# Performance work log

Hardware: AMD Instinct MI355X
Metric: run time of the kernel (lower is better)

## Reference

```python
import jax, jax.numpy as jnp
import numpy as np

DIM = 1024
NUM_HEADS = 16
HEAD_DIM = DIM // NUM_HEADS


def setup_inputs() -> dict:
    key = jax.random.key(0)
    k_x, k_wqkv, k_bqkv, k_wo, k_bo = jax.random.split(key, 5)
    scale = DIM ** -0.5
    return {
        "x": jax.random.normal(k_x, (4, 2048, DIM), dtype=jnp.float32),
        "w_qkv": jax.random.normal(k_wqkv, (DIM, 3 * DIM), dtype=jnp.float32) * scale,
        "b_qkv": jax.random.normal(k_bqkv, (3 * DIM,), dtype=jnp.float32) * 0.02,
        "w_out": jax.random.normal(k_wo, (DIM, DIM), dtype=jnp.float32) * scale,
        "b_out": jax.random.normal(k_bo, (DIM,), dtype=jnp.float32) * 0.02,
    }


def reference(x, w_qkv, b_qkv, w_out, b_out):
    B, S, D = x.shape
    H, Hd = NUM_HEADS, HEAD_DIM
    # QKV projection: (B,S,3D) -> (3,B,H,S,Hd)
    qkv = (x @ w_qkv + b_qkv).reshape(B, S, 3, H, Hd).transpose(2, 0, 3, 1, 4)
    q, k, v = qkv[0], qkv[1], qkv[2]
    scores = jnp.einsum('bhqd,bhkd->bhqk', q, k) / (Hd ** 0.5)
    attn = jax.nn.softmax(scores, axis=-1)  # dropout is identity in eval
    out = jnp.einsum('bhqk,bhkd->bhqd', attn, v)
    out = out.transpose(0, 2, 1, 3).reshape(B, S, D)
    return out @ w_out + b_out
```

## Files before the change

kernel.cpp:

```cpp
#include <hip/hip_runtime.h>
#include <hip/hip_bf16.h>
#include <stdint.h>

#define SEQ 2048
#define DIM 1024
#define NH 16
#define HD 64

typedef __attribute__((ext_vector_type(8))) short short8;
typedef __attribute__((ext_vector_type(4))) float f32x4;
typedef __attribute__((ext_vector_type(4))) float float4v;
typedef __attribute__((ext_vector_type(4))) unsigned short u16x4;
typedef __attribute__((ext_vector_type(2))) unsigned int u32x2;

#define MFMA16(a, b, c) __builtin_amdgcn_mfma_f32_16x16x32_bf16(a, b, c, 0, 0, 0)

#define QSCALE 0.1803368801111244f
#define LOG2_THR 11.0f

__device__ __forceinline__ unsigned short f2b(float f) {
  union { float f; unsigned int u; } x; x.f = f;
  unsigned int r = (x.u + 0x7FFFu + ((x.u >> 16) & 1u)) >> 16;
  return (unsigned short)r;
}

__device__ __forceinline__ float exp2v(float x) {
  float r;
  asm("v_exp_f32 %0, %1" : "=v"(r) : "v"(x));
  return r;
}

__device__ __forceinline__ unsigned int pk2(float a, float b) {
  __hip_bfloat162 h = __float22bfloat162_rn(float2{a, b});
  union { __hip_bfloat162 h; unsigned int u; } c; c.h = h;
  return c.u;
}

__device__ __forceinline__ void gld16(const void* g, void* l) {
  __builtin_amdgcn_global_load_lds(
      (const __attribute__((address_space(1))) unsigned int*)(uintptr_t)g,
      (__attribute__((address_space(3))) unsigned int*)(unsigned int)(uintptr_t)l,
      16, 0, 0);
}

__global__ void cast_bf16_kernel(const float* __restrict__ in,
                                 unsigned short* __restrict__ out, int n4) {
  int stride = gridDim.x * blockDim.x;
  for (int i = blockIdx.x * blockDim.x + threadIdx.x; i < n4; i += stride) {
    float4v v = *(const float4v*)(in + (size_t)i * 4);
    u16x4 o;
    o.x = f2b(v.x); o.y = f2b(v.y); o.z = f2b(v.z); o.w = f2b(v.w);
    *(u16x4*)(out + (size_t)i * 4) = o;
  }
}

__global__ void transpose_cast_kernel(const float* __restrict__ in,
                                      unsigned short* __restrict__ out,
                                      int rows, int cols) {
  __shared__ float tile[32][33];
  const int t = threadIdx.x, tx = t & 31, ty = t >> 5;
  const int c0 = blockIdx.x * 32, r0 = blockIdx.y * 32;
#pragma unroll
  for (int j = 0; j < 4; j++)
    tile[ty + 8 * j][tx] = in[(size_t)(r0 + ty + 8 * j) * cols + c0 + tx];
  __syncthreads();
#pragma unroll
  for (int j = 0; j < 4; j++)
    out[(size_t)(c0 + ty + 8 * j) * rows + r0 + tx] = f2b(tile[tx][ty + 8 * j]);
}

template <int EPI>
__global__ __launch_bounds__(256, 2) void gemm_bt_kernel(
    const unsigned short* __restrict__ A, const unsigned short* __restrict__ Bt,
    const float* __restrict__ bias, float* __restrict__ Cf,
    int M, int N, int K,
    unsigned short* __restrict__ Qb, unsigned short* __restrict__ Kb,
    unsigned short* __restrict__ Vt) {
  __shared__ unsigned short lA[128 * 32];
  __shared__ unsigned short lB[128 * 32];
  const int t = threadIdx.x, lane = t & 63, w = t >> 6;
  const int l15 = lane & 15, lg = lane >> 4;
  const int wr = (w >> 1) * 64, wc = (w & 1) * 64;
  const int bm = blockIdx.x, bn = blockIdx.y;
  const char* Ag = (const char*)(A + (size_t)bm * 128 * K);
  const char* Bg = (const char*)(Bt + (size_t)bn * 128 * K);
  const int sr = t >> 2;
  const int sc = (t & 3) * 16;
  const size_t rowb = (size_t)K * 2;

  f32x4 acc[4][4];
#pragma unroll
  for (int m = 0; m < 4; m++)
#pragma unroll
    for (int n = 0; n < 4; n++) acc[m][n] = (f32x4){0.f, 0.f, 0.f, 0.f};

  for (int k0 = 0; k0 < K; k0 += 32) {
    __syncthreads();
    const size_t kbyte = (size_t)k0 * 2;
    gld16(Ag + (size_t)sr * rowb + kbyte + sc, &lA[t * 8]);
    gld16(Ag + (size_t)(sr + 64) * rowb + kbyte + sc, &lA[2048 + t * 8]);
    gld16(Bg + (size_t)sr * rowb + kbyte + sc, &lB[t * 8]);
    gld16(Bg + (size_t)(sr + 64) * rowb + kbyte + sc, &lB[2048 + t * 8]);
    asm volatile("s_waitcnt vmcnt(0)" ::: "memory");
    __syncthreads();
    short8 af[4], bf_[4];
#pragma unroll
    for (int m = 0; m < 4; m++)
      af[m] = *(const short8*)&lA[(wr + m * 16 + l15) * 32 + lg * 8];
#pragma unroll
    for (int n = 0; n < 4; n++)
      bf_[n] = *(const short8*)&lB[(wc + n * 16 + l15) * 32 + lg * 8];
#pragma unroll
    for (int m = 0; m < 4; m++)
#pragma unroll
      for (int n = 0; n < 4; n++)
        acc[m][n] = MFMA16(af[m], bf_[n], acc[m][n]);
  }

#pragma unroll
  for (int m = 0; m < 4; m++) {
#pragma unroll
    for (int n = 0; n < 4; n++) {
      const int row0 = bm * 128 + wr + m * 16 + lg * 4;
      const int col = bn * 128 + wc + n * 16 + l15;
      const float bv = bias[col];
      if (EPI == 1) {
#pragma unroll
        for (int rr = 0; rr < 4; rr++)
          Cf[(size_t)(row0 + rr) * N + col] = acc[m][n][rr] + bv;
      } else {
        const int three = col >> 10, rem = col & 1023;
        const int h = rem >> 6, d = rem & 63;
        const int b = row0 >> 11, s0 = row0 & 2047;
        const size_t bh = (size_t)(b * NH + h);
        if (three == 0) {
#pragma unroll
          for (int rr = 0; rr < 4; rr++)
            Qb[(bh * SEQ + s0 + rr) * HD + d] = f2b((acc[m][n][rr] + bv) * QSCALE);
        } else if (three == 1) {
#pragma unroll
          for (int rr = 0; rr < 4; rr++)
            Kb[(bh * SEQ + s0 + rr) * HD + d] = f2b(acc[m][n][rr] + bv);
        } else {
          u16x4 pk;
#pragma unroll
          for (int rr = 0; rr < 4; rr++) pk[rr] = f2b(acc[m][n][rr] + bv);
          *(u16x4*)&Vt[(bh * HD + d) * SEQ + s0] = pk;
        }
      }
    }
  }
}

__global__ __launch_bounds__(256, 3) void attn_kernel(
    const unsigned short* __restrict__ Qb, const unsigned short* __restrict__ Kb,
    const unsigned short* __restrict__ Vt, unsigned short* __restrict__ AO) {
  __shared__ unsigned short kT[2][64 * 64];
  __shared__ unsigned short vT[2][64 * 64];
  __shared__ unsigned short pT[4][32 * 64];
  const int t = threadIdx.x, lane = t & 63, w = t >> 6;
  const int l15 = lane & 15, lg = lane >> 4;
  const int flat = blockIdx.y * 16 + blockIdx.x;
  const int xcd = flat & 7, j = flat >> 3;
  const int bh = xcd * 8 + (j >> 4);
  const int q0 = (j & 15) * 128;
  const char* Qg = (const char*)(Qb + (size_t)bh * SEQ * HD);
  const char* Kg = (const char*)(Kb + (size_t)bh * SEQ * HD);
  const char* Vg = (const char*)(Vt + (size_t)bh * HD * SEQ);

  short8 qa[2][2];
#pragma unroll
  for (int h = 0; h < 2; h++) {
    const char* qrow = Qg + (size_t)(q0 + w * 32 + h * 16 + l15) * 128;
    qa[h][0] = *(const short8*)(qrow + lg * 16);
    qa[h][1] = *(const short8*)(qrow + 64 + lg * 16);
  }

  f32x4 o[2][4];
#pragma unroll
  for (int h = 0; h < 2; h++)
#pragma unroll
    for (int n = 0; n < 4; n++) o[h][n] = (f32x4){0.f, 0.f, 0.f, 0.f};
  float m_r[2] = {-1e30f, -1e30f}, l_r[2] = {0.f, 0.f};

  const int sr0 = t >> 3;
  const int scx = (t & 7) * 16;

#define STAGE(buf, kv0_)                                                               \
  do {                                                                                 \
    const int r0_ = sr0, r1_ = sr0 + 32;                                               \
    gld16(Kg + (size_t)((kv0_) + r0_) * 128 + (scx ^ ((r0_ & 7) << 4)),                \
          &kT[buf][t * 8]);                                                            \
    gld16(Kg + (size_t)((kv0_) + r1_) * 128 + (scx ^ ((r1_ & 7) << 4)),                \
          &kT[buf][2048 + t * 8]);                                                     \
    gld16(Vg + (size_t)r0_ * (SEQ * 2) + (size_t)(kv0_) * 2 + (scx ^ ((r0_ & 7) << 4)),\
          &vT[buf][t * 8]);                                                            \
    gld16(Vg + (size_t)r1_ * (SEQ * 2) + (size_t)(kv0_) * 2 + (scx ^ ((r1_ & 7) << 4)),\
          &vT[buf][2048 + t * 8]);                                                     \
  } while (0)

  STAGE(0, 0);
  asm volatile("s_waitcnt vmcnt(0)" ::: "memory");
  __syncthreads();
  int cur = 0;

  for (int kv0 = 0; kv0 < SEQ; kv0 += 64) {
    if (kv0 + 64 < SEQ) STAGE(cur ^ 1, kv0 + 64);

    const char* kb = (const char*)&kT[cur][0];
    f32x4 s[2][4];
#pragma unroll
    for (int h = 0; h < 2; h++)
#pragma unroll
      for (int n = 0; n < 4; n++) s[h][n] = (f32x4){0.f, 0.f, 0.f, 0.f};
    __builtin_amdgcn_s_setprio(1);
#pragma unroll
    for (int n = 0; n < 4; n++) {
      const int row = n * 16 + l15;
      const char* kr = kb + row * 128;
      const int sw = (row & 7) << 4;
      short8 a0 = *(const short8*)(kr + ((lg * 16) ^ sw));
      short8 a1 = *(const short8*)(kr + ((64 + lg * 16) ^ sw));
      s[0][n] = MFMA16(a0, qa[0][0], s[0][n]);
      s[0][n] = MFMA16(a1, qa[0][1], s[0][n]);
      s[1][n] = MFMA16(a0, qa[1][0], s[1][n]);
      s[1][n] = MFMA16(a1, qa[1][1], s[1][n]);
    }
    __builtin_amdgcn_s_setprio(0);

    float mx[2];
#pragma unroll
    for (int h = 0; h < 2; h++) {
      float m0 = fmaxf(fmaxf(s[h][0][0], s[h][0][1]), fmaxf(s[h][0][2], s[h][0][3]));
#pragma unroll
      for (int n = 1; n < 4; n++) {
        m0 = fmaxf(m0, fmaxf(fmaxf(s[h][n][0], s[h][n][1]), fmaxf(s[h][n][2], s[h][n][3])));
      }
      m0 = fmaxf(m0, __shfl_xor(m0, 16, 64));
      m0 = fmaxf(m0, __shfl_xor(m0, 32, 64));
      mx[h] = m0;
    }

    const int grow = (mx[0] > m_r[0] + LOG2_THR) | (mx[1] > m_r[1] + LOG2_THR);
    if (__any(grow)) {
      float al[2];
#pragma unroll
      for (int h = 0; h < 2; h++) {
        const float nm = fmaxf(m_r[h], mx[h]);
        al[h] = exp2v(m_r[h] - nm);
        m_r[h] = nm;
        l_r[h] *= al[h];
      }
#pragma unroll
      for (int h = 0; h < 2; h++)
#pragma unroll
        for (int r = 0; r < 4; r++) {
          const float alb = __shfl(al[h], lg * 4 + r, 64);
#pragma unroll
          for (int n = 0; n < 4; n++) o[h][n][r] *= alb;
        }
    }

    char* pb = (char*)&pT[w][0];
    const int swp = (l15 & 7) << 4;
#pragma unroll
    for (int h = 0; h < 2; h++) {
      float rs = 0.f;
#pragma unroll
      for (int n = 0; n < 4; n++) {
#pragma unroll
        for (int r = 0; r < 4; r++) {
          const float p = exp2v(s[h][n][r] - m_r[h]);
          s[h][n][r] = p;
          rs += p;
        }
        u32x2 c;
        c.x = pk2(s[h][n][0], s[h][n][1]);
        c.y = pk2(s[h][n][2], s[h][n][3]);
        *(u32x2*)(pb + (h * 16 + l15) * 128 + ((n * 32 + lg * 8) ^ swp)) = c;
      }
      rs += __shfl_xor(rs, 16, 64);
      rs += __shfl_xor(rs, 32, 64);
      l_r[h] += rs;
    }
    short8 pa[2][2];
#pragma unroll
    for (int h = 0; h < 2; h++) {
      const char* pr = pb + (h * 16 + l15) * 128;
      pa[h][0] = *(const short8*)(pr + ((lg * 16) ^ swp));
      pa[h][1] = *(const short8*)(pr + ((64 + lg * 16) ^ swp));
    }

    const char* vb = (const char*)&vT[cur][0];
    __builtin_amdgcn_s_setprio(1);
#pragma unroll
    for (int n = 0; n < 4; n++) {
      const int row = n * 16 + l15;
      const char* vr = vb + row * 128;
      const int sw = (row & 7) << 4;
      short8 b0 = *(const short8*)(vr + ((lg * 16) ^ sw));
      short8 b1 = *(const short8*)(vr + ((64 + lg * 16) ^ sw));
      o[0][n] = MFMA16(pa[0][0], b0, o[0][n]);
      o[0][n] = MFMA16(pa[0][1], b1, o[0][n]);
      o[1][n] = MFMA16(pa[1][0], b0, o[1][n]);
      o[1][n] = MFMA16(pa[1][1], b1, o[1][n]);
    }
    __builtin_amdgcn_s_setprio(0);

    asm volatile("s_waitcnt vmcnt(0)" ::: "memory");
    __syncthreads();
    cur ^= 1;
  }
#undef STAGE

  float inv[2];
#pragma unroll
  for (int h = 0; h < 2; h++) inv[h] = 1.f / l_r[h];
  const int b = bh >> 4, hh = bh & 15;
  unsigned short* aob = AO + (size_t)b * SEQ * DIM + (size_t)hh * HD;
#pragma unroll
  for (int h = 0; h < 2; h++)
#pragma unroll
    for (int r = 0; r < 4; r++) {
      const float lb = __shfl(inv[h], lg * 4 + r, 64);
      const int s_ = q0 + w * 32 + h * 16 + lg * 4 + r;
#pragma unroll
      for (int n = 0; n < 4; n++) {
        const int d_ = n * 16 + l15;
        aob[(size_t)s_ * DIM + d_] = f2b(o[h][n][r] * lb);
      }
    }
}

extern "C" void kernel_launch(void* const* d_in, const int* in_sizes, int n_in,
                              void* d_out, int out_size, void* d_ws, size_t ws_size,
                              hipStream_t stream) {
  const float* x = (const float*)d_in[0];
  const float* w_qkv = (const float*)d_in[1];
  const float* b_qkv = (const float*)d_in[2];
  const float* w_out = (const float*)d_in[3];
  const float* b_out = (const float*)d_in[4];
  float* out = (float*)d_out;

  char* ws = (char*)d_ws;
  unsigned short* xb    = (unsigned short*)(ws);
  unsigned short* wqkvT = (unsigned short*)(ws + (16u << 20));
  unsigned short* woT   = (unsigned short*)(ws + (22u << 20));
  unsigned short* Qb    = (unsigned short*)(ws + (24u << 20));
  unsigned short* Kb    = (unsigned short*)(ws + (40u << 20));
  unsigned short* Vt    = (unsigned short*)(ws + (56u << 20));
  unsigned short* AO    = (unsigned short*)(ws + (72u << 20));

  const int M = 4 * SEQ;

  cast_bf16_kernel<<<2048, 256, 0, stream>>>(x, xb, M * DIM / 4);
  transpose_cast_kernel<<<dim3(3 * DIM / 32, DIM / 32), 256, 0, stream>>>(w_qkv, wqkvT, DIM, 3 * DIM);
  transpose_cast_kernel<<<dim3(DIM / 32, DIM / 32), 256, 0, stream>>>(w_out, woT, DIM, DIM);

  gemm_bt_kernel<0><<<dim3(M / 128, 3 * DIM / 128), 256, 0, stream>>>(
      xb, wqkvT, b_qkv, nullptr, M, 3 * DIM, DIM, Qb, Kb, Vt);

  attn_kernel<<<dim3(SEQ / 128, 4 * NH), 256, 0, stream>>>(Qb, Kb, Vt, AO);

  gemm_bt_kernel<1><<<dim3(M / 128, DIM / 128), 256, 0, stream>>>(
      AO, woT, b_out, out, M, DIM, DIM, nullptr, nullptr, nullptr);
}
```

Measured before the change: 300.7 us.

## Load K and V tiles directly from global memory instead of LDS staging

```diff
diff --git a/kernel.cpp b/kernel.cpp
--- a/kernel.cpp
+++ b/kernel.cpp
@@ -152,12 +152,10 @@
   }
 }
 
-__global__ __launch_bounds__(256, 3) void attn_kernel(
+__global__ __launch_bounds__(256, 4) void attn_kernel(
     const unsigned short* __restrict__ Qb, const unsigned short* __restrict__ Kb,
     const unsigned short* __restrict__ Vt, unsigned short* __restrict__ AO) {
-  __shared__ unsigned short kT[2][64 * 64];
-  __shared__ unsigned short vT[2][64 * 64];
-  __shared__ unsigned short pT[4][32 * 64];
+  __shared__ unsigned short pT[4][16 * 64];
   const int t = threadIdx.x, lane = t & 63, w = t >> 6;
   const int l15 = lane & 15, lg = lane >> 4;
   const int flat = blockIdx.y * 16 + blockIdx.x;
@@ -183,31 +181,7 @@
     for (int n = 0; n < 4; n++) o[h][n] = (f32x4){0.f, 0.f, 0.f, 0.f};
   float m_r[2] = {-1e30f, -1e30f}, l_r[2] = {0.f, 0.f};
 
-  const int sr0 = t >> 3;
-  const int scx = (t & 7) * 16;
-
-#define STAGE(buf, kv0_)                                                               \
-  do {                                                                                 \
-    const int r0_ = sr0, r1_ = sr0 + 32;                                               \
-    gld16(Kg + (size_t)((kv0_) + r0_) * 128 + (scx ^ ((r0_ & 7) << 4)),                \
-          &kT[buf][t * 8]);                                                            \
-    gld16(Kg + (size_t)((kv0_) + r1_) * 128 + (scx ^ ((r1_ & 7) << 4)),                \
-          &kT[buf][2048 + t * 8]);                                                     \
-    gld16(Vg + (size_t)r0_ * (SEQ * 2) + (size_t)(kv0_) * 2 + (scx ^ ((r0_ & 7) << 4)),\
-          &vT[buf][t * 8]);                                                            \
-    gld16(Vg + (size_t)r1_ * (SEQ * 2) + (size_t)(kv0_) * 2 + (scx ^ ((r1_ & 7) << 4)),\
-          &vT[buf][2048 + t * 8]);                                                     \
-  } while (0)
-
-  STAGE(0, 0);
-  asm volatile("s_waitcnt vmcnt(0)" ::: "memory");
-  __syncthreads();
-  int cur = 0;
-
   for (int kv0 = 0; kv0 < SEQ; kv0 += 64) {
-    if (kv0 + 64 < SEQ) STAGE(cur ^ 1, kv0 + 64);
-
-    const char* kb = (const char*)&kT[cur][0];
     f32x4 s[2][4];
 #pragma unroll
     for (int h = 0; h < 2; h++)
@@ -216,11 +190,9 @@
     __builtin_amdgcn_s_setprio(1);
 #pragma unroll
     for (int n = 0; n < 4; n++) {
-      const int row = n * 16 + l15;
-      const char* kr = kb + row * 128;
-      const int sw = (row & 7) << 4;
-      short8 a0 = *(const short8*)(kr + ((lg * 16) ^ sw));
-      short8 a1 = *(const short8*)(kr + ((64 + lg * 16) ^ sw));
+      const char* kr = Kg + (size_t)(kv0 + n * 16 + l15) * 128;
+      short8 a0 = *(const short8*)(kr + lg * 16);
+      short8 a1 = *(const short8*)(kr + 64 + lg * 16);
       s[0][n] = MFMA16(a0, qa[0][0], s[0][n]);
       s[0][n] = MFMA16(a1, qa[0][1], s[0][n]);
       s[1][n] = MFMA16(a0, qa[1][0], s[1][n]);
@@ -263,6 +235,7 @@
 
     char* pb = (char*)&pT[w][0];
     const int swp = (l15 & 7) << 4;
+    short8 pa[2][2];
 #pragma unroll
     for (int h = 0; h < 2; h++) {
       float rs = 0.f;
@@ -277,41 +250,29 @@
         u32x2 c;
         c.x = pk2(s[h][n][0], s[h][n][1]);
         c.y = pk2(s[h][n][2], s[h][n][3]);
-        *(u32x2*)(pb + (h * 16 + l15) * 128 + ((n * 32 + lg * 8) ^ swp)) = c;
+        *(u32x2*)(pb + l15 * 128 + ((n * 32 + lg * 8) ^ swp)) = c;
       }
       rs += __shfl_xor(rs, 16, 64);
       rs += __shfl_xor(rs, 32, 64);
       l_r[h] += rs;
-    }
-    short8 pa[2][2];
-#pragma unroll
-    for (int h = 0; h < 2; h++) {
-      const char* pr = pb + (h * 16 + l15) * 128;
+      const char* pr = pb + l15 * 128;
       pa[h][0] = *(const short8*)(pr + ((lg * 16) ^ swp));
       pa[h][1] = *(const short8*)(pr + ((64 + lg * 16) ^ swp));
     }
 
-    const char* vb = (const char*)&vT[cur][0];
     __builtin_amdgcn_s_setprio(1);
 #pragma unroll
     for (int n = 0; n < 4; n++) {
-      const int row = n * 16 + l15;
-      const char* vr = vb + row * 128;
-      const int sw = (row & 7) << 4;
-      short8 b0 = *(const short8*)(vr + ((lg * 16) ^ sw));
-      short8 b1 = *(const short8*)(vr + ((64 + lg * 16) ^ sw));
+      const char* vr = Vg + (size_t)(n * 16 + l15) * (SEQ * 2) + (size_t)kv0 * 2;
+      short8 b0 = *(const short8*)(vr + lg * 16);
+      short8 b1 = *(const short8*)(vr + 64 + lg * 16);
       o[0][n] = MFMA16(pa[0][0], b0, o[0][n]);
       o[0][n] = MFMA16(pa[0][1], b1, o[0][n]);
       o[1][n] = MFMA16(pa[1][0], b0, o[1][n]);
       o[1][n] = MFMA16(pa[1][1], b1, o[1][n]);
     }
     __builtin_amdgcn_s_setprio(0);
-
-    asm volatile("s_waitcnt vmcnt(0)" ::: "memory");
-    __syncthreads();
-    cur ^= 1;
-  }
-#undef STAGE
+  }
 
   float inv[2];
 #pragma unroll
```

After: 420.1 us. 1.4x slower.
